# Performance work log

Hardware: AMD Instinct MI355X
Metric: run time of the kernel (lower is better)

## Reference

```python
import jax, jax.numpy as jnp
import numpy as np

N, E, D = 50000, 800000, 128   # nodes, edges, input feat dim
H, C = 4, 32                   # heads, per-head channels (H*C = 128)
OUT = 128                      # final linear out_channels
NEG_SLOPE = 0.2


def _glorot(k, shape):
    fan = shape[0] + shape[-1]
    return jax.random.normal(k, shape, jnp.float32) * np.float32(np.sqrt(2.0 / fan))


def setup_inputs() -> dict:
    key = jax.random.key(0)
    ks = jax.random.split(key, 16)
    HC = H * C
    z = lambda n: jnp.zeros((n,), jnp.float32)
    return {
        "x": jax.random.normal(ks[0], (N, D), jnp.float32),
        "edge_index": jax.random.randint(ks[1], (2, E), 0, N),
        "edge_attr": jax.random.uniform(ks[2], (E, 1), jnp.float32),
        # GATv2 layer 1 (in = D)
        "Wl1": _glorot(ks[3], (D, HC)), "bl1": z(HC),
        "Wr1": _glorot(ks[4], (D, HC)), "br1": z(HC),
        "We1": _glorot(ks[5], (1, HC)),
        "att1": _glorot(ks[6], (H, C)),
        "bo1": z(HC),
        # GATv2 layer 2 (in = H*C)
        "Wl2": _glorot(ks[7], (HC, HC)), "bl2": z(HC),
        "Wr2": _glorot(ks[8], (HC, HC)), "br2": z(HC),
        "We2": _glorot(ks[9], (1, HC)),
        "att2": _glorot(ks[10], (H, C)),
        "bo2": z(HC),
        # final Linear
        "Wlin": _glorot(ks[11], (HC, OUT)), "blin": z(OUT),
    }


def _segment_softmax(logits, seg, n):
    # logits: [E_tot, H], seg: [E_tot] target node ids
    m = jax.ops.segment_max(logits, seg, num_segments=n)          # [N, H]
    m = jnp.where(jnp.isfinite(m), m, 0.0)                         # empty-segment guard
    e = jnp.exp(logits - m[seg])
    s = jax.ops.segment_sum(e, seg, num_segments=n)                # [N, H]
    return e / (s[seg] + 1e-16)


def _gatv2_layer(x, src, dst, eattr, Wl, bl, Wr, br, We, att, bo):
    n = x.shape[0]
    xl = (x @ Wl + bl).reshape(n, H, C)   # source transform (lin_l)
    xr = (x @ Wr + br).reshape(n, H, C)   # target transform (lin_r)
    ee = (eattr @ We).reshape(-1, H, C)   # edge transform (lin_edge)
    m = jax.nn.leaky_relu(xl[src] + xr[dst] + ee, NEG_SLOPE)       # [E_tot, H, C]
    logits = jnp.einsum('ehc,hc->eh', m, att)                      # [E_tot, H]
    alpha = _segment_softmax(logits, dst, n)                       # [E_tot, H]
    out = jax.ops.segment_sum(xl[src] * alpha[..., None], dst, num_segments=n)
    return out.reshape(n, H * C) + bo


def _with_self_loops(edge_index, edge_attr, n):
    # PyG add_self_loops(fill_value='mean'): loop attr = mean of incoming edge attrs
    src, dst = edge_index[0], edge_index[1]
    sums = jax.ops.segment_sum(edge_attr, dst, num_segments=n)     # [N, 1]
    cnts = jax.ops.segment_sum(jnp.ones((edge_attr.shape[0], 1), edge_attr.dtype),
                               dst, num_segments=n)
    loop_attr = jnp.where(cnts > 0, sums / jnp.maximum(cnts, 1.0), 0.0)
    ar = jnp.arange(n, dtype=src.dtype)
    full_src = jnp.concatenate([src, ar])
    full_dst = jnp.concatenate([dst, ar])
    full_attr = jnp.concatenate([edge_attr, loop_attr], axis=0)
    return full_src, full_dst, full_attr


def reference(x, edge_index, edge_attr,
              Wl1, bl1, Wr1, br1, We1, att1, bo1,
              Wl2, bl2, Wr2, br2, We2, att2, bo2,
              Wlin, blin):
    x = x.astype(jnp.float32)
    edge_attr = edge_attr.astype(jnp.float32)
    src, dst, eattr = _with_self_loops(edge_index, edge_attr, x.shape[0])
    h = jax.nn.relu(_gatv2_layer(x, src, dst, eattr, Wl1, bl1, Wr1, br1, We1, att1, bo1))
    h = jax.nn.relu(_gatv2_layer(h, src, dst, eattr, Wl2, bl2, Wr2, br2, We2, att2, bo2))
    return jax.nn.relu(h @ Wlin + blin)
```

## Files before the change

kernel.cpp:

```cpp
#include <hip/hip_runtime.h>
#include <hip/hip_fp16.h>
#include <math.h>

#define NEG 0.2f
#define CNT_SHIFT 42
#define SUM_MASK ((1ULL << CNT_SHIFT) - 1)
#define ROWS 48

typedef _Float16 hf2 __attribute__((ext_vector_type(2)));
typedef _Float16 hf8 __attribute__((ext_vector_type(8)));
typedef float f4 __attribute__((ext_vector_type(4)));

template <int CTRL>
__device__ __forceinline__ float dpp_radd(float x) {
  int t = __builtin_amdgcn_update_dpp(0, __float_as_int(x), CTRL, 0xf, 0xf,
                                      false);
  return x + __int_as_float(t);
}

__device__ __forceinline__ uint4 pack_wline(const float* __restrict__ W,
                                            int L) {
  int lane = L & 63, nt = (L >> 6) & 7, kc = L >> 9;
  int kbase = kc * 32 + (lane >> 4) * 8;
  int col = nt * 16 + (lane & 15);
  const float* wp = W + (size_t)kbase * 128 + col;
  uint4 pk;
  pk.x = __builtin_bit_cast(unsigned, __builtin_amdgcn_cvt_pkrtz(wp[0], wp[128]));
  pk.y = __builtin_bit_cast(unsigned, __builtin_amdgcn_cvt_pkrtz(wp[256], wp[384]));
  pk.z = __builtin_bit_cast(unsigned, __builtin_amdgcn_cvt_pkrtz(wp[512], wp[640]));
  pk.w = __builtin_bit_cast(unsigned, __builtin_amdgcn_cvt_pkrtz(wp[768], wp[896]));
  return pk;
}

__device__ __forceinline__ hf2 gat_node(int v, const hf2* __restrict__ xl,
    const hf2* __restrict__ xr, const unsigned* __restrict__ edge,
    const unsigned long long* __restrict__ hist, hf2 weh, hf2 atth, hf2 negh,
    const float* __restrict__ bo, int lane, int n) {
  int ch = lane * 2;
  hf2 xrh = xr[(size_t)v * 64 + lane];
  unsigned long long hv = hist[v];
  int cnt = (int)(hv >> CNT_SHIFT);
  int cntc = cnt < ROWS ? cnt : ROWS;
  const unsigned* erow = edge + (size_t)v * ROWS;

  float denom[2] = {0.f, 0.f};
  float ac0[2] = {0.f, 0.f}, ac1[2] = {0.f, 0.f};

  int full = cntc & ~7;
  for (int ofs = 0; ofs < full; ofs += 8) {
    const unsigned* ep = erow + ofs;
    unsigned rec[8];
#pragma unroll
    for (int j = 0; j < 8; ++j) rec[j] = ep[j];
    hf2 xv[8];
#pragma unroll
    for (int j = 0; j < 8; ++j)
      xv[j] = xl[(size_t)(rec[j] & 0xffffu) * 64 + lane];
    float p[8];
#pragma unroll
    for (int j = 0; j < 8; ++j) {
      hf2 eah = __builtin_bit_cast(hf2, (rec[j] >> 16) * 0x10001u);
      hf2 t = (xv[j] + xrh) + eah * weh;
      hf2 tn = t * negh;
      t = __builtin_elementwise_max(t, tn);
      p[j] = __builtin_amdgcn_fdot2(t, atth, 0.f, false);
    }
#pragma unroll
    for (int j = 0; j < 8; ++j) {
      p[j] = dpp_radd<0xB1>(p[j]);
      p[j] = dpp_radd<0x4E>(p[j]);
      p[j] = dpp_radd<0x141>(p[j]);
      p[j] = dpp_radd<0x140>(p[j]);
    }
#pragma unroll
    for (int j = 0; j < 8; ++j) {
      float w = __builtin_amdgcn_exp2f(p[j]);
      denom[j & 1] += w;
      ac0[j & 1] = fmaf(w, (float)xv[j].x, ac0[j & 1]);
      ac1[j & 1] = fmaf(w, (float)xv[j].y, ac1[j & 1]);
    }
  }
  if (full < cntc) {
    const unsigned* ep = erow + full;
    unsigned rec[8];
#pragma unroll
    for (int j = 0; j < 8; ++j) rec[j] = ep[j];
    hf2 xv[8];
#pragma unroll
    for (int j = 0; j < 8; ++j) {
      unsigned si = rec[j] & 0xffffu;
      si = si < (unsigned)n ? si : 0u;
      xv[j] = xl[(size_t)si * 64 + lane];
    }
    float p[8];
#pragma unroll
    for (int j = 0; j < 8; ++j) {
      hf2 eah = __builtin_bit_cast(hf2, (rec[j] >> 16) * 0x10001u);
      hf2 t = (xv[j] + xrh) + eah * weh;
      hf2 tn = t * negh;
      t = __builtin_elementwise_max(t, tn);
      p[j] = __builtin_amdgcn_fdot2(t, atth, 0.f, false);
    }
#pragma unroll
    for (int j = 0; j < 8; ++j) {
      p[j] = dpp_radd<0xB1>(p[j]);
      p[j] = dpp_radd<0x4E>(p[j]);
      p[j] = dpp_radd<0x141>(p[j]);
      p[j] = dpp_radd<0x140>(p[j]);
    }
#pragma unroll
    for (int j = 0; j < 8; ++j) {
      float w = (full + j < cntc) ? __builtin_amdgcn_exp2f(p[j]) : 0.f;
      denom[j & 1] += w;
      ac0[j & 1] = fmaf(w, (float)xv[j].x, ac0[j & 1]);
      ac1[j & 1] = fmaf(w, (float)xv[j].y, ac1[j & 1]);
    }
  }
  {
    float sumf = (float)(hv & SUM_MASK) * 2.3283064365386963e-10f;
    float mean = cnt > 0 ? sumf / (float)cnt : 0.f;
    hf2 xself = xl[(size_t)v * 64 + lane];
    _Float16 mh = (_Float16)mean;
    hf2 meanh = {mh, mh};
    hf2 t = (xself + xrh) + meanh * weh;
    hf2 tn = t * negh;
    t = __builtin_elementwise_max(t, tn);
    float ps = __builtin_amdgcn_fdot2(t, atth, 0.f, false);
    ps = dpp_radd<0xB1>(ps);
    ps = dpp_radd<0x4E>(ps);
    ps = dpp_radd<0x141>(ps);
    ps = dpp_radd<0x140>(ps);
    float w = __builtin_amdgcn_exp2f(ps);
    denom[0] += w;
    ac0[0] = fmaf(w, (float)xself.x, ac0[0]);
    ac1[0] = fmaf(w, (float)xself.y, ac1[0]);
  }
  float rden = 1.0f / (denom[0] + denom[1] + 1e-16f);
  int ch0 = ch;
  float o0 = fmaxf(fmaf(ac0[0] + ac0[1], rden, bo[ch0]), 0.f);
  float o1 = fmaxf(fmaf(ac1[0] + ac1[1], rden, bo[ch0 + 1]), 0.f);
  hf2 oh = {(_Float16)o0, (_Float16)o1};
  return oh;
}

__global__ __launch_bounds__(256, 2) void k_fuse1(
    const float* __restrict__ X, const float* __restrict__ Wa,
    const float* __restrict__ Wb, const float* __restrict__ Ba,
    const float* __restrict__ Bb, hf2* __restrict__ Y0, hf2* __restrict__ Y1,
    int nrows, int gGemm, const int* __restrict__ ei,
    const float* __restrict__ eattr, unsigned long long* __restrict__ hist,
    unsigned* __restrict__ edge, int E, int nbP,
    const float* __restrict__ W2a, const float* __restrict__ W2b,
    const float* __restrict__ W2c, uint4* __restrict__ wout) {
  __shared__ uint4 Wl[2][1024];
  int bid = blockIdx.x, tid = threadIdx.x;

  if (bid < gGemm) {
    int lane = tid & 63, wid = tid >> 6;
    int quad = lane >> 4, rl = lane & 15;
    int rbase = bid * 128 + wid * 32;

    hf8 a[4][2];
#pragma unroll
    for (int rs = 0; rs < 2; ++rs) {
      int gr = rbase + rs * 16 + rl;
      gr = gr < nrows ? gr : nrows - 1;
      const float* xp = X + (size_t)gr * 128 + quad * 8;
#pragma unroll
      for (int kc = 0; kc < 4; ++kc) {
        float4 u = *reinterpret_cast<const float4*>(xp + kc * 32);
        float4 u2 = *reinterpret_cast<const float4*>(xp + kc * 32 + 4);
        uint4 pk;
        pk.x = __builtin_bit_cast(unsigned, __builtin_amdgcn_cvt_pkrtz(u.x, u.y));
        pk.y = __builtin_bit_cast(unsigned, __builtin_amdgcn_cvt_pkrtz(u.z, u.w));
        pk.z = __builtin_bit_cast(unsigned, __builtin_amdgcn_cvt_pkrtz(u2.x, u2.y));
        pk.w = __builtin_bit_cast(unsigned, __builtin_amdgcn_cvt_pkrtz(u2.z, u2.w));
        a[kc][rs] = __builtin_bit_cast(hf8, pk);
      }
    }

    f4 acc[2][2][8];
#pragma unroll
    for (int m = 0; m < 2; ++m)
#pragma unroll
      for (int rs = 0; rs < 2; ++rs)
#pragma unroll
        for (int nt = 0; nt < 8; ++nt) acc[m][rs][nt] = (f4)0.f;

#pragma unroll
    for (int h = 0; h < 2; ++h) {
      __syncthreads();
#pragma unroll
      for (int m = 0; m < 2; ++m) {
        const float* W = m ? Wb : Wa;
        for (int i = tid; i < 1024; i += 256)
          Wl[m][i] = pack_wline(W, h * 1024 + i);
      }
      __syncthreads();
#pragma unroll
      for (int kcl = 0; kcl < 2; ++kcl) {
        int kc = h * 2 + kcl;
#pragma unroll
        for (int nt = 0; nt < 8; ++nt) {
#pragma unroll
          for (int m = 0; m < 2; ++m) {
            hf8 w = __builtin_bit_cast(hf8,
                Wl[m][(kcl * 8 + nt) * 64 + lane]);
            acc[m][0][nt] = __builtin_amdgcn_mfma_f32_16x16x32_f16(
                w, a[kc][0], acc[m][0][nt], 0, 0, 0);
            acc[m][1][nt] = __builtin_amdgcn_mfma_f32_16x16x32_f16(
                w, a[kc][1], acc[m][1][nt], 0, 0, 0);
          }
        }
      }
    }

#pragma unroll
    for (int m = 0; m < 2; ++m) {
      const float* Bb_ = m ? Bb : Ba;
      hf2* Yv = m ? Y1 : Y0;
#pragma unroll
      for (int rs = 0; rs < 2; ++rs) {
        int row = rbase + rs * 16 + rl;
        if (row < nrows) {
#pragma unroll
          for (int nt = 0; nt < 8; ++nt) {
            f4 av = acc[m][rs][nt];
            int col = nt * 16 + quad * 4;
            float4 bb = *reinterpret_cast<const float4*>(&Bb_[col]);
            float o0 = av[0] + bb.x, o1 = av[1] + bb.y;
            float o2 = av[2] + bb.z, o3 = av[3] + bb.w;
            unsigned p0 = __builtin_bit_cast(unsigned,
                __builtin_amdgcn_cvt_pkrtz(o0, o1));
            unsigned p1 = __builtin_bit_cast(unsigned,
                __builtin_amdgcn_cvt_pkrtz(o2, o3));
            *reinterpret_cast<uint2*>((_Float16*)Yv + (size_t)row * 128 + col)
                = make_uint2(p0, p1);
          }
        }
      }
    }
  } else if (bid < gGemm + nbP) {
    int e0 = (bid - gGemm) * 4096 + tid;
    int d[16], s[16];
    float ea[16];
    bool valid[16];
#pragma unroll
    for (int j = 0; j < 16; ++j) {
      int e = e0 + j * 256;
      valid[j] = e < E;
      int ec = valid[j] ? e : 0;
      d[j] = ei[E + ec];
      s[j] = ei[ec];
      ea[j] = eattr[ec];
    }
#pragma unroll
    for (int j = 0; j < 16; ++j) {
      if (valid[j]) {
        unsigned long long fx =
            (unsigned long long)(ea[j] * 4294967296.0f);
        unsigned long long old =
            atomicAdd(&hist[d[j]], (1ULL << CNT_SHIFT) + fx);
        int rank = (int)(old >> CNT_SHIFT);
        _Float16 h = (_Float16)ea[j];
        unsigned hb = (unsigned)__builtin_bit_cast(unsigned short, h);
        if (rank < ROWS)
          edge[(size_t)d[j] * ROWS + rank] = (unsigned)s[j] | (hb << 16);
      }
    }
  } else {
    int gid = (bid - gGemm - nbP) * 256 + tid;
    if (gid < 3 * 2048) {
      int mat = gid >> 11;
      const float* W = mat == 0 ? W2a : mat == 1 ? W2b : W2c;
      wout[gid] = pack_wline(W, gid & 2047);
    }
  }
}

__global__ __launch_bounds__(256) void k_gatg(const hf2* __restrict__ xl,
    const hf2* __restrict__ xr, const unsigned* __restrict__ edge,
    const unsigned long long* __restrict__ hist, const float* __restrict__ We,
    const float* __restrict__ att, const float* __restrict__ bo,
    const uint4* __restrict__ Wp0, const uint4* __restrict__ Wp1,
    const float* __restrict__ B0, const float* __restrict__ B1,
    hf2* __restrict__ out0, hf2* __restrict__ out1, int n) {
  __shared__ _Float16 hbuf[16][136];
  int tid = threadIdx.x;
  int lane = tid & 63, wid = tid >> 6;
  int quad = lane >> 4, rl = lane & 15;
  int base = blockIdx.x * 16;
  int ch = lane * 2;
  hf2 weh = {(_Float16)We[ch], (_Float16)We[ch + 1]};
  hf2 atth = {(_Float16)(att[ch] * 1.44269504f),
              (_Float16)(att[ch + 1] * 1.44269504f)};
  hf2 negh = {(_Float16)NEG, (_Float16)NEG};

#pragma unroll 1
  for (int i = 0; i < 4; ++i) {
    int row = wid * 4 + i;
    int v = base + row;
    hf2 oh = {(_Float16)0.f, (_Float16)0.f};
    if (v < n)
      oh = gat_node(v, xl, xr, edge, hist, weh, atth, negh, bo, lane, n);
    *reinterpret_cast<hf2*>(&hbuf[row][2 * lane]) = oh;
  }
  __syncthreads();

  hf8 hfrag[4];
#pragma unroll
  for (int kc = 0; kc < 4; ++kc)
    hfrag[kc] = *reinterpret_cast<const hf8*>(&hbuf[rl][kc * 32 + quad * 8]);

#pragma unroll
  for (int ntl = 0; ntl < 2; ++ntl) {
    int nt = wid * 2 + ntl;
#pragma unroll
    for (int m = 0; m < 2; ++m) {
      const uint4* Wp = m ? Wp1 : Wp0;
      f4 a = (f4)0.f;
#pragma unroll
      for (int kc = 0; kc < 4; ++kc) {
        hf8 w = __builtin_bit_cast(hf8, Wp[(kc * 8 + nt) * 64 + lane]);
        a = __builtin_amdgcn_mfma_f32_16x16x32_f16(w, hfrag[kc], a, 0, 0, 0);
      }
      int col = nt * 16 + quad * 4;
      const float* Bb = m ? B1 : B0;
      float4 bb = *reinterpret_cast<const float4*>(&Bb[col]);
      float o0 = a[0] + bb.x, o1 = a[1] + bb.y;
      float o2 = a[2] + bb.z, o3 = a[3] + bb.w;
      hf2 h0 = {(_Float16)o0, (_Float16)o1};
      hf2 h1 = {(_Float16)o2, (_Float16)o3};
      int row = base + rl;
      if (row < n) {
        hf2* outp = m ? out1 : out0;
        uint2 pk = make_uint2(__builtin_bit_cast(unsigned, h0),
                              __builtin_bit_cast(unsigned, h1));
        *reinterpret_cast<uint2*>(outp + (size_t)row * 64 + nt * 8 + quad * 2)
            = pk;
      }
    }
  }
}

__global__ __launch_bounds__(256) void k_gat(const hf2* __restrict__ xl,
    const hf2* __restrict__ xr, const unsigned* __restrict__ edge,
    const unsigned long long* __restrict__ hist, const float* __restrict__ We,
    const float* __restrict__ att, const float* __restrict__ bo,
    hf2* __restrict__ out, int n) {
  int lane = threadIdx.x & 63;
  int wid = threadIdx.x >> 6;
  int v = blockIdx.x * 4 + wid;
  if (v >= n) return;
  int ch = lane * 2;
  hf2 weh = {(_Float16)We[ch], (_Float16)We[ch + 1]};
  hf2 atth = {(_Float16)(att[ch] * 1.44269504f),
              (_Float16)(att[ch + 1] * 1.44269504f)};
  hf2 negh = {(_Float16)NEG, (_Float16)NEG};
  hf2 oh = gat_node(v, xl, xr, edge, hist, weh, atth, negh, bo, lane, n);
  out[(size_t)v * 64 + lane] = oh;
}

__global__ __launch_bounds__(256, 2) void k_gemmf(
    const _Float16* __restrict__ X, const uint4* __restrict__ Wp0,
    const float* __restrict__ B0, float* __restrict__ Y, int nrows) {
  __shared__ uint4 Wl[2048];
  int tid = threadIdx.x;
  for (int i = tid; i < 2048; i += 256) Wl[i] = Wp0[i];

  int lane = tid & 63, wid = tid >> 6;
  int quad = lane >> 4, rl = lane & 15;
  int rbase = blockIdx.x * 128 + wid * 32;

  hf8 a[4][2];
#pragma unroll
  for (int rs = 0; rs < 2; ++rs) {
    int gr = rbase + rs * 16 + rl;
    gr = gr < nrows ? gr : nrows - 1;
    const _Float16* xp = X + (size_t)gr * 128 + quad * 8;
#pragma unroll
    for (int kc = 0; kc < 4; ++kc)
      a[kc][rs] = *reinterpret_cast<const hf8*>(xp + kc * 32);
  }

  f4 acc[2][8];
#pragma unroll
  for (int rs = 0; rs < 2; ++rs)
#pragma unroll
    for (int nt = 0; nt < 8; ++nt) acc[rs][nt] = (f4)0.f;

  __syncthreads();

#pragma unroll
  for (int kc = 0; kc < 4; ++kc) {
#pragma unroll
    for (int nt = 0; nt < 8; ++nt) {
      hf8 w = __builtin_bit_cast(hf8, Wl[(kc * 8 + nt) * 64 + lane]);
      acc[0][nt] = __builtin_amdgcn_mfma_f32_16x16x32_f16(
          w, a[kc][0], acc[0][nt], 0, 0, 0);
      acc[1][nt] = __builtin_amdgcn_mfma_f32_16x16x32_f16(
          w, a[kc][1], acc[1][nt], 0, 0, 0);
    }
  }

#pragma unroll
  for (int rs = 0; rs < 2; ++rs) {
    int row = rbase + rs * 16 + rl;
    if (row < nrows) {
#pragma unroll
      for (int nt = 0; nt < 8; ++nt) {
        f4 av = acc[rs][nt];
        int col = nt * 16 + quad * 4;
        float4 bb = *reinterpret_cast<const float4*>(&B0[col]);
        float o0 = fmaxf(av[0] + bb.x, 0.f);
        float o1 = fmaxf(av[1] + bb.y, 0.f);
        float o2 = fmaxf(av[2] + bb.z, 0.f);
        float o3 = fmaxf(av[3] + bb.w, 0.f);
        *reinterpret_cast<float4*>(&Y[(size_t)row * 128 + col]) =
            make_float4(o0, o1, o2, o3);
      }
    }
  }
}

extern "C" void kernel_launch(void* const* d_in, const int* in_sizes, int n_in,
                              void* d_out, int out_size, void* d_ws, size_t ws_size,
                              hipStream_t stream) {
  const float* x     = (const float*)d_in[0];
  const int*   ei    = (const int*)d_in[1];
  const float* eattr = (const float*)d_in[2];
  const float* Wl1 = (const float*)d_in[3];
  const float* bl1 = (const float*)d_in[4];
  const float* Wr1 = (const float*)d_in[5];
  const float* br1 = (const float*)d_in[6];
  const float* We1 = (const float*)d_in[7];
  const float* att1 = (const float*)d_in[8];
  const float* bo1 = (const float*)d_in[9];
  const float* Wl2 = (const float*)d_in[10];
  const float* bl2 = (const float*)d_in[11];
  const float* Wr2 = (const float*)d_in[12];
  const float* br2 = (const float*)d_in[13];
  const float* We2 = (const float*)d_in[14];
  const float* att2 = (const float*)d_in[15];
  const float* bo2 = (const float*)d_in[16];
  const float* Wlin = (const float*)d_in[17];
  const float* blin = (const float*)d_in[18];
  float* out = (float*)d_out;

  const int N = in_sizes[0] / 128;
  const int E = in_sizes[1] / 2;

  hf2* xl = (hf2*)d_ws;
  hf2* xr = xl + (size_t)N * 64;
  hf2* h16 = xr + (size_t)N * 64;
  uint4* w16 = (uint4*)(h16 + (size_t)N * 64);
  unsigned long long* hist = (unsigned long long*)(w16 + 3 * 2048);
  unsigned* edge = (unsigned*)(hist + N);

  hf2* xl2 = (hf2*)d_out;
  hf2* xr2 = xl2 + (size_t)N * 64;

  (void)hipMemsetAsync(hist, 0, sizeof(unsigned long long) * (size_t)N,
                       stream);

  int gGemm = (N + 127) / 128;
  int nbP = (E + 4095) / 4096;
  int gGat = (N + 3) / 4;
  int gGatg = (N + 15) / 16;

  k_fuse1<<<gGemm + nbP + 24, 256, 0, stream>>>(x, Wl1, Wr1, bl1, br1,
      xl, xr, N, gGemm, ei, eattr, hist, edge, E, nbP,
      Wl2, Wr2, Wlin, w16);

  k_gatg<<<gGatg, 256, 0, stream>>>(xl, xr, edge, hist, We1, att1, bo1,
      w16, w16 + 2048, bl2, br2, xl2, xr2, N);

  k_gat<<<gGat, 256, 0, stream>>>(xl2, xr2, edge, hist, We2, att2, bo2,
                                  h16, N);

  k_gemmf<<<gGemm, 256, 0, stream>>>((const _Float16*)h16, w16 + 2 * 2048,
                                     blin, out, N);
}
```

Before: 271.1 us.

## Fuse layer-2 aggregation with final linear and widen GAT blocks to 512

```diff
diff --git a/kernel.cpp b/kernel.cpp
--- a/kernel.cpp
+++ b/kernel.cpp
@@ -136,9 +136,8 @@
     ac1[0] = fmaf(w, (float)xself.y, ac1[0]);
   }
   float rden = 1.0f / (denom[0] + denom[1] + 1e-16f);
-  int ch0 = ch;
-  float o0 = fmaxf(fmaf(ac0[0] + ac0[1], rden, bo[ch0]), 0.f);
-  float o1 = fmaxf(fmaf(ac1[0] + ac1[1], rden, bo[ch0 + 1]), 0.f);
+  float o0 = fmaxf(fmaf(ac0[0] + ac0[1], rden, bo[ch]), 0.f);
+  float o1 = fmaxf(fmaf(ac1[0] + ac1[1], rden, bo[ch + 1]), 0.f);
   hf2 oh = {(_Float16)o0, (_Float16)o1};
   return oh;
 }
@@ -278,7 +277,7 @@
   }
 }
 
-__global__ __launch_bounds__(256) void k_gatg(const hf2* __restrict__ xl,
+__global__ __launch_bounds__(512) void k_gatg(const hf2* __restrict__ xl,
     const hf2* __restrict__ xr, const unsigned* __restrict__ edge,
     const unsigned long long* __restrict__ hist, const float* __restrict__ We,
     const float* __restrict__ att, const float* __restrict__ bo,
@@ -297,8 +296,8 @@
   hf2 negh = {(_Float16)NEG, (_Float16)NEG};
 
 #pragma unroll 1
-  for (int i = 0; i < 4; ++i) {
-    int row = wid * 4 + i;
+  for (int i = 0; i < 2; ++i) {
+    int row = wid * 2 + i;
     int v = base + row;
     hf2 oh = {(_Float16)0.f, (_Float16)0.f};
     if (v < n)
@@ -312,115 +311,84 @@
   for (int kc = 0; kc < 4; ++kc)
     hfrag[kc] = *reinterpret_cast<const hf8*>(&hbuf[rl][kc * 32 + quad * 8]);
 
-#pragma unroll
-  for (int ntl = 0; ntl < 2; ++ntl) {
-    int nt = wid * 2 + ntl;
-#pragma unroll
-    for (int m = 0; m < 2; ++m) {
-      const uint4* Wp = m ? Wp1 : Wp0;
-      f4 a = (f4)0.f;
-#pragma unroll
-      for (int kc = 0; kc < 4; ++kc) {
-        hf8 w = __builtin_bit_cast(hf8, Wp[(kc * 8 + nt) * 64 + lane]);
-        a = __builtin_amdgcn_mfma_f32_16x16x32_f16(w, hfrag[kc], a, 0, 0, 0);
-      }
-      int col = nt * 16 + quad * 4;
-      const float* Bb = m ? B1 : B0;
-      float4 bb = *reinterpret_cast<const float4*>(&Bb[col]);
-      float o0 = a[0] + bb.x, o1 = a[1] + bb.y;
-      float o2 = a[2] + bb.z, o3 = a[3] + bb.w;
-      hf2 h0 = {(_Float16)o0, (_Float16)o1};
-      hf2 h1 = {(_Float16)o2, (_Float16)o3};
-      int row = base + rl;
-      if (row < n) {
-        hf2* outp = m ? out1 : out0;
-        uint2 pk = make_uint2(__builtin_bit_cast(unsigned, h0),
-                              __builtin_bit_cast(unsigned, h1));
-        *reinterpret_cast<uint2*>(outp + (size_t)row * 64 + nt * 8 + quad * 2)
-            = pk;
-      }
-    }
-  }
-}
-
-__global__ __launch_bounds__(256) void k_gat(const hf2* __restrict__ xl,
+  int nt = wid;
+#pragma unroll
+  for (int m = 0; m < 2; ++m) {
+    const uint4* Wp = m ? Wp1 : Wp0;
+    f4 a = (f4)0.f;
+#pragma unroll
+    for (int kc = 0; kc < 4; ++kc) {
+      hf8 w = __builtin_bit_cast(hf8, Wp[(kc * 8 + nt) * 64 + lane]);
+      a = __builtin_amdgcn_mfma_f32_16x16x32_f16(w, hfrag[kc], a, 0, 0, 0);
+    }
+    int col = nt * 16 + quad * 4;
+    const float* Bb = m ? B1 : B0;
+    float4 bb = *reinterpret_cast<const float4*>(&Bb[col]);
+    float o0 = a[0] + bb.x, o1 = a[1] + bb.y;
+    float o2 = a[2] + bb.z, o3 = a[3] + bb.w;
+    hf2 h0 = {(_Float16)o0, (_Float16)o1};
+    hf2 h1 = {(_Float16)o2, (_Float16)o3};
+    int row = base + rl;
+    if (row < n) {
+      hf2* outp = m ? out1 : out0;
+      uint2 pk = make_uint2(__builtin_bit_cast(unsigned, h0),
+                            __builtin_bit_cast(unsigned, h1));
+      *reinterpret_cast<uint2*>(outp + (size_t)row * 64 + nt * 8 + quad * 2)
+          = pk;
+    }
+  }
+}
+
+__global__ __launch_bounds__(512) void k_gatgf(const hf2* __restrict__ xl,
     const hf2* __restrict__ xr, const unsigned* __restrict__ edge,
     const unsigned long long* __restrict__ hist, const float* __restrict__ We,
     const float* __restrict__ att, const float* __restrict__ bo,
-    hf2* __restrict__ out, int n) {
-  int lane = threadIdx.x & 63;
-  int wid = threadIdx.x >> 6;
-  int v = blockIdx.x * 4 + wid;
-  if (v >= n) return;
+    const uint4* __restrict__ Wp0, const float* __restrict__ B0,
+    float* __restrict__ outf, int n) {
+  __shared__ _Float16 hbuf[16][136];
+  int tid = threadIdx.x;
+  int lane = tid & 63, wid = tid >> 6;
+  int quad = lane >> 4, rl = lane & 15;
+  int base = blockIdx.x * 16;
   int ch = lane * 2;
   hf2 weh = {(_Float16)We[ch], (_Float16)We[ch + 1]};
   hf2 atth = {(_Float16)(att[ch] * 1.44269504f),
               (_Float16)(att[ch + 1] * 1.44269504f)};
   hf2 negh = {(_Float16)NEG, (_Float16)NEG};
-  hf2 oh = gat_node(v, xl, xr, edge, hist, weh, atth, negh, bo, lane, n);
-  out[(size_t)v * 64 + lane] = oh;
-}
-
-__global__ __launch_bounds__(256, 2) void k_gemmf(
-    const _Float16* __restrict__ X, const uint4* __restrict__ Wp0,
-    const float* __restrict__ B0, float* __restrict__ Y, int nrows) {
-  __shared__ uint4 Wl[2048];
-  int tid = threadIdx.x;
-  for (int i = tid; i < 2048; i += 256) Wl[i] = Wp0[i];
-
-  int lane = tid & 63, wid = tid >> 6;
-  int quad = lane >> 4, rl = lane & 15;
-  int rbase = blockIdx.x * 128 + wid * 32;
-
-  hf8 a[4][2];
-#pragma unroll
-  for (int rs = 0; rs < 2; ++rs) {
-    int gr = rbase + rs * 16 + rl;
-    gr = gr < nrows ? gr : nrows - 1;
-    const _Float16* xp = X + (size_t)gr * 128 + quad * 8;
-#pragma unroll
-    for (int kc = 0; kc < 4; ++kc)
-      a[kc][rs] = *reinterpret_cast<const hf8*>(xp + kc * 32);
-  }
-
-  f4 acc[2][8];
-#pragma unroll
-  for (int rs = 0; rs < 2; ++rs)
-#pragma unroll
-    for (int nt = 0; nt < 8; ++nt) acc[rs][nt] = (f4)0.f;
-
+
+#pragma unroll 1
+  for (int i = 0; i < 2; ++i) {
+    int row = wid * 2 + i;
+    int v = base + row;
+    hf2 oh = {(_Float16)0.f, (_Float16)0.f};
+    if (v < n)
+      oh = gat_node(v, xl, xr, edge, hist, weh, atth, negh, bo, lane, n);
+    *reinterpret_cast<hf2*>(&hbuf[row][2 * lane]) = oh;
+  }
   __syncthreads();
 
+  hf8 hfrag[4];
+#pragma unroll
+  for (int kc = 0; kc < 4; ++kc)
+    hfrag[kc] = *reinterpret_cast<const hf8*>(&hbuf[rl][kc * 32 + quad * 8]);
+
+  int nt = wid;
+  f4 a = (f4)0.f;
 #pragma unroll
   for (int kc = 0; kc < 4; ++kc) {
-#pragma unroll
-    for (int nt = 0; nt < 8; ++nt) {
-      hf8 w = __builtin_bit_cast(hf8, Wl[(kc * 8 + nt) * 64 + lane]);
-      acc[0][nt] = __builtin_amdgcn_mfma_f32_16x16x32_f16(
-          w, a[kc][0], acc[0][nt], 0, 0, 0);
-      acc[1][nt] = __builtin_amdgcn_mfma_f32_16x16x32_f16(
-          w, a[kc][1], acc[1][nt], 0, 0, 0);
-    }
-  }
-
-#pragma unroll
-  for (int rs = 0; rs < 2; ++rs) {
-    int row = rbase + rs * 16 + rl;
-    if (row < nrows) {
-#pragma unroll
-      for (int nt = 0; nt < 8; ++nt) {
-        f4 av = acc[rs][nt];
-        int col = nt * 16 + quad * 4;
-        float4 bb = *reinterpret_cast<const float4*>(&B0[col]);
-        float o0 = fmaxf(av[0] + bb.x, 0.f);
-        float o1 = fmaxf(av[1] + bb.y, 0.f);
-        float o2 = fmaxf(av[2] + bb.z, 0.f);
-        float o3 = fmaxf(av[3] + bb.w, 0.f);
-        *reinterpret_cast<float4*>(&Y[(size_t)row * 128 + col]) =
-            make_float4(o0, o1, o2, o3);
-      }
-    }
-  }
+    hf8 w = __builtin_bit_cast(hf8, Wp0[(kc * 8 + nt) * 64 + lane]);
+    a = __builtin_amdgcn_mfma_f32_16x16x32_f16(w, hfrag[kc], a, 0, 0, 0);
+  }
+  int col = nt * 16 + quad * 4;
+  float4 bb = *reinterpret_cast<const float4*>(&B0[col]);
+  float o0 = fmaxf(a[0] + bb.x, 0.f);
+  float o1 = fmaxf(a[1] + bb.y, 0.f);
+  float o2 = fmaxf(a[2] + bb.z, 0.f);
+  float o3 = fmaxf(a[3] + bb.w, 0.f);
+  int row = base + rl;
+  if (row < n)
+    *reinterpret_cast<float4*>(&outf[(size_t)row * 128 + col]) =
+        make_float4(o0, o1, o2, o3);
 }
 
 extern "C" void kernel_launch(void* const* d_in, const int* in_sizes, int n_in,
@@ -459,25 +427,25 @@
 
   hf2* xl2 = (hf2*)d_out;
   hf2* xr2 = xl2 + (size_t)N * 64;
+  float* outf = (float*)d_ws;
 
   (void)hipMemsetAsync(hist, 0, sizeof(unsigned long long) * (size_t)N,
                        stream);
 
   int gGemm = (N + 127) / 128;
   int nbP = (E + 4095) / 4096;
-  int gGat = (N + 3) / 4;
   int gGatg = (N + 15) / 16;
 
   k_fuse1<<<gGemm + nbP + 24, 256, 0, stream>>>(x, Wl1, Wr1, bl1, br1,
       xl, xr, N, gGemm, ei, eattr, hist, edge, E, nbP,
       Wl2, Wr2, Wlin, w16);
 
-  k_gatg<<<gGatg, 256, 0, stream>>>(xl, xr, edge, hist, We1, att1, bo1,
+  k_gatg<<<gGatg, 512, 0, stream>>>(xl, xr, edge, hist, We1, att1, bo1,
       w16, w16 + 2048, bl2, br2, xl2, xr2, N);
 
-  k_gat<<<gGat, 256, 0, stream>>>(xl2, xr2, edge, hist, We2, att2, bo2,
-                                  h16, N);
-
-  k_gemmf<<<gGemm, 256, 0, stream>>>((const _Float16*)h16, w16 + 2 * 2048,
-                                     blin, out, N);
-}
+  k_gatgf<<<gGatg, 512, 0, stream>>>(xl2, xr2, edge, hist, We2, att2, bo2,
+      w16 + 2 * 2048, blin, outf, N);
+
+  (void)hipMemcpyAsync(out, outf, (size_t)N * 128 * sizeof(float),
+                       hipMemcpyDeviceToDevice, stream);
+}
```

Measured after the change: 277.0 us. +2.2%, slower.
